# Performance work log

Hardware: AMD Instinct MI355X
Metric: run time of the kernel (lower is better)

Reference implementation:

```python
import jax, jax.numpy as jnp
import numpy as np
from jax import lax

DIM = 256
SEQ = 1024
BATCH = 4
EPS = 1e-6
P_TANH_SCALE = 10.0


def setup_inputs() -> dict:
    key = jax.random.key(0)
    ks = jax.random.split(key, 12)
    d, n, b = DIM, SEQ, BATCH
    half = d // 2
    x = jax.random.normal(ks[0], (b, n, d), jnp.float32)
    # RoPE frequencies (standard llama-style), complex freqs_cis split into cos/sin
    inv_freq = 1.0 / (10000.0 ** (np.arange(half, dtype=np.float64) * 2.0 / d))
    ang = np.outer(np.arange(n, dtype=np.float64), inv_freq)  # (n, d/2)
    freqs_cis_cos = jnp.asarray(np.cos(ang), jnp.float32)
    freqs_cis_sin = jnp.asarray(np.sin(ang), jnp.float32)
    s = 1.0 / np.sqrt(d)
    Wqkv = jax.random.normal(ks[1], (3 * d, d), jnp.float32) * s
    qconv_w = jax.random.normal(ks[2], (d, 4), jnp.float32) * 0.3
    qconv_b = jax.random.normal(ks[3], (d,), jnp.float32) * 0.02
    kconv_w = jax.random.normal(ks[4], (d, 4), jnp.float32) * 0.3
    kconv_b = jax.random.normal(ks[5], (d,), jnp.float32) * 0.02
    vconv_w = jax.random.normal(ks[6], (d, 4), jnp.float32) * 0.3
    vconv_b = jax.random.normal(ks[7], (d,), jnp.float32) * 0.02
    Wparam = jax.random.normal(ks[8], (2, d), jnp.float32) * s
    bparam = jnp.zeros((2,), jnp.float32)
    W0 = jnp.eye(d, dtype=jnp.float32)  # nn.init.eye_
    Wgate = jax.random.normal(ks[9], (d, d), jnp.float32) * s
    Wout = jax.random.normal(ks[10], (d, d), jnp.float32) * s
    return dict(x=x, freqs_cis_cos=freqs_cis_cos, freqs_cis_sin=freqs_cis_sin,
                Wqkv=Wqkv, qconv_w=qconv_w, qconv_b=qconv_b,
                kconv_w=kconv_w, kconv_b=kconv_b, vconv_w=vconv_w, vconv_b=vconv_b,
                Wparam=Wparam, bparam=bparam, W0=W0, Wgate=Wgate, Wout=Wout)


def _causal_dwconv(x, w, bias):
    # x: (b,n,d); w: (d,4); torch Conv1d(k=4, pad=3, groups=d) truncated to [:n]
    # y[t] = sum_j w[:,j] * x[t-3+j]  (zero left-pad)
    b, n, d = x.shape
    xp = jnp.pad(x, ((0, 0), (3, 0), (0, 0)))
    y = sum(xp[:, j:j + n, :] * w[None, None, :, j] for j in range(4))
    return y + bias[None, None, :]


def _rope(x, cos, sin):
    # x: (b,n,d); pairs (x[...,2i], x[...,2i+1]) rotated by freqs_cis
    xr, xi = x[..., 0::2], x[..., 1::2]
    c, s = cos[None], sin[None]
    outr = xr * c - xi * s
    outi = xr * s + xi * c
    return jnp.stack((outr, outi), axis=-1).reshape(x.shape)


def _l2norm(x):
    nrm = jnp.linalg.norm(x, axis=-1, keepdims=True)
    return x / jnp.maximum(nrm, 1e-12)


def _forward(x, cos, sin, Wqkv, qw, qb, kw, kb, vw, vb, Wparam, bparam, W0, Wgate, Wout):
    b, n, d = x.shape
    qkv = x @ Wqkv.T
    q, k, v = jnp.split(qkv, 3, axis=-1)
    q = _causal_dwconv(q, qw, qb)
    k = _causal_dwconv(k, kw, kb)
    v = _causal_dwconv(v, vw, vb)
    q = _l2norm(_rope(q, cos, sin))
    k = _l2norm(_rope(k, cos, sin))
    params = x @ Wparam.T + bparam  # (b,n,2)
    eta = jax.nn.sigmoid(params[..., 0])    # (b,n)
    alpha = jax.nn.sigmoid(params[..., 1])  # (b,n)

    def step(carry, inp):
        A, W = carry                      # (b,d,d)
        qt, kt, vt, et, at = inp          # (b,d)x3, (b,)x2
        pred = jnp.einsum('bd,bde->be', kt, W)
        diff = pred - vt
        grad_pred = 3.0 * jnp.tanh(P_TANH_SCALE * diff) * (diff * diff)  # p == 3
        grad_W = kt[:, :, None] * grad_pred[:, None, :]
        A = at[:, None, None] * A - et[:, None, None] * grad_W
        a4 = jnp.square(jnp.square(A))  # q == 4
        denom = jnp.sqrt(a4.sum(axis=(-2, -1), keepdims=True)) + EPS
        W = A / denom
        yt = jnp.einsum('bd,bde->be', qt, W)
        return (A, W), yt

    A0 = jnp.zeros((b, d, d), x.dtype)
    W_init = jnp.broadcast_to(W0, (b, d, d)).astype(x.dtype)
    xs = (q.transpose(1, 0, 2), k.transpose(1, 0, 2), v.transpose(1, 0, 2),
          eta.T, alpha.T)
    _, yT = lax.scan(jax.checkpoint(step), (A0, W_init), xs)
    y = yT.transpose(1, 0, 2)  # (b,n,d)
    return (y @ Wout.T) * jax.nn.sigmoid(x @ Wgate.T)


def reference(x, freqs_cis_cos, freqs_cis_sin, Wqkv, qconv_w, qconv_b,
              kconv_w, kconv_b, vconv_w, vconv_b, Wparam, bparam, W0, Wgate, Wout):
    return _forward(x, freqs_cis_cos, freqs_cis_sin, Wqkv, qconv_w, qconv_b,
                    kconv_w, kconv_b, vconv_w, vconv_b, Wparam, bparam, W0, Wgate, Wout)
```

## Files before the change

### kernel.cpp

```cpp
#include <hip/hip_runtime.h>

#define DIMD 256
#define SEQT 1024
#define NB   4
#define RBS  36

typedef float v2f __attribute__((ext_vector_type(2)));
#define FMA2(a,b,c) __builtin_elementwise_fma((a),(b),(c))

__device__ __forceinline__ float sigmoidf_(float x){ return 1.0f/(1.0f+expf(-x)); }

template<int EPI>
__global__ __launch_bounds__(256) void gemm_bt(const float* __restrict__ A,
    const float* __restrict__ Bm, float* __restrict__ C, int N,
    const float* __restrict__ gpre)
{
  __shared__ float sA[64][68];
  __shared__ float sB[64][68];
  const int nb = N >> 6;
  const int bm = blockIdx.x / nb, bn = blockIdx.x - bm*nb;
  const int m0 = bm << 6, n0 = bn << 6;
  const int tid = threadIdx.x;
  const int tr = tid >> 4, tc = tid & 15;
  float acc[4][4];
  #pragma unroll
  for (int i=0;i<4;i++)
    #pragma unroll
    for (int j=0;j<4;j++) acc[i][j]=0.f;

  for (int kc=0;kc<4;kc++){
    __syncthreads();
    for (int i=tid;i<1024;i+=256){
      int r = i >> 4, q4 = i & 15;
      *(float4*)&sA[r][q4*4] = ((const float4*)(A  + (m0+r)*256 + kc*64))[q4];
      *(float4*)&sB[r][q4*4] = ((const float4*)(Bm + (n0+r)*256 + kc*64))[q4];
    }
    __syncthreads();
    #pragma unroll
    for (int kq=0;kq<16;kq++){
      float4 av[4], bv[4];
      #pragma unroll
      for (int i=0;i<4;i++) av[i] = *(const float4*)&sA[tr+16*i][kq*4];
      #pragma unroll
      for (int j=0;j<4;j++) bv[j] = *(const float4*)&sB[tc+16*j][kq*4];
      #pragma unroll
      for (int i=0;i<4;i++)
        #pragma unroll
        for (int j=0;j<4;j++)
          acc[i][j] = fmaf(av[i].x,bv[j].x, fmaf(av[i].y,bv[j].y,
                      fmaf(av[i].z,bv[j].z, fmaf(av[i].w,bv[j].w, acc[i][j]))));
    }
  }
  #pragma unroll
  for (int i=0;i<4;i++){
    #pragma unroll
    for (int j=0;j<4;j++){
      int m = m0 + tr + 16*i, n = n0 + tc + 16*j;
      float val = acc[i][j];
      if (EPI==1) val *= sigmoidf_(gpre[m*N+n]);
      C[m*N+n] = val;
    }
  }
}

__global__ __launch_bounds__(256) void prep_kernel(
    const float* __restrict__ qkvr, const float* __restrict__ x,
    const float* __restrict__ cosT, const float* __restrict__ sinT,
    const float* __restrict__ qw, const float* __restrict__ qbias,
    const float* __restrict__ kw, const float* __restrict__ kbias,
    const float* __restrict__ vw, const float* __restrict__ vbias,
    const float* __restrict__ Wparam, const float* __restrict__ bparam,
    float* __restrict__ qo, float* __restrict__ ko, float* __restrict__ vo,
    float* __restrict__ eo, float* __restrict__ ao)
{
  const int bt = blockIdx.x;
  const int t = bt & 1023;
  const int d = threadIdx.x;

  float4 wq = ((const float4*)qw)[d];
  float4 wk = ((const float4*)kw)[d];
  float4 wv = ((const float4*)vw)[d];
  const float wqj[4] = {wq.x,wq.y,wq.z,wq.w};
  const float wkj[4] = {wk.x,wk.y,wk.z,wk.w};
  const float wvj[4] = {wv.x,wv.y,wv.z,wv.w};
  float qa = qbias[d], ka = kbias[d], va = vbias[d];
  #pragma unroll
  for (int j=0;j<4;j++){
    int tt = t - 3 + j;
    if (tt >= 0) {
      const float* row = qkvr + (size_t)(bt - 3 + j) * 768;
      qa = fmaf(row[d],      wqj[j], qa);
      ka = fmaf(row[256+d],  wkj[j], ka);
      va = fmaf(row[512+d],  wvj[j], va);
    }
  }
  vo[bt*256 + d] = va;

  __shared__ float sq[256], sk[256];
  __shared__ float red[4][4];
  sq[d] = qa; sk[d] = ka;
  __syncthreads();
  const int i = d >> 1;
  const float c = cosT[t*128 + i], s = sinT[t*128 + i];
  float qr, krp;
  if ((d & 1) == 0) { qr = sq[d]*c - sq[d+1]*s;  krp = sk[d]*c - sk[d+1]*s; }
  else              { qr = sq[d-1]*s + sq[d]*c;  krp = sk[d-1]*s + sk[d]*c; }

  const float xd = x[bt*256 + d];
  float r0 = qr*qr, r1 = krp*krp, r2 = xd*Wparam[d], r3 = xd*Wparam[256+d];
  #pragma unroll
  for (int m=1;m<64;m<<=1){
    r0 += __shfl_xor(r0, m, 64);
    r1 += __shfl_xor(r1, m, 64);
    r2 += __shfl_xor(r2, m, 64);
    r3 += __shfl_xor(r3, m, 64);
  }
  const int w = d >> 6;
  if ((d & 63) == 0){ red[w][0]=r0; red[w][1]=r1; red[w][2]=r2; red[w][3]=r3; }
  __syncthreads();
  float qss = red[0][0]+red[1][0]+red[2][0]+red[3][0];
  float kss = red[0][1]+red[1][1]+red[2][1]+red[3][1];
  qo[bt*256+d] = qr  / fmaxf(sqrtf(qss), 1e-12f);
  ko[bt*256+d] = krp / fmaxf(sqrtf(kss), 1e-12f);
  if (d == 0){
    float p0 = red[0][2]+red[1][2]+red[2][2]+red[3][2] + bparam[0];
    float p1 = red[0][3]+red[1][3]+red[2][3]+red[3][3] + bparam[1];
    eo[bt] = 1.f/(1.f+expf(-p0));
    ao[bt] = 1.f/(1.f+expf(-p1));
  }
}

__global__ __launch_bounds__(1024, 4) void scan_kernel(
    const float* __restrict__ qn, const float* __restrict__ kn,
    const float* __restrict__ vn, const float* __restrict__ eta,
    const float* __restrict__ alpha, const float* __restrict__ W0,
    float* __restrict__ y, float* __restrict__ g_s4)
{
  const int blkid = blockIdx.x;
  const int b     = blkid >> 1;
  const int h     = blkid & 1;
  const int peerb = blkid ^ 1;
  const int tid = threadIdx.x;
  const int rg = tid & 7;
  const int cl = tid >> 3;
  const int cg = (h << 7) + cl;
  const int r0 = rg << 5;
  const int koff = rg * RBS;

  __shared__ float s_k[3][8*RBS], s_q[3][8*RBS], s_v[3][256];
  __shared__ float s_ea[3][2];
  __shared__ float s_acc[4];
  __shared__ unsigned s_cnt[4];

  v2f A2[16];
  #pragma unroll
  for (int j=0;j<16;j++) A2[j] = (v2f)(0.f);

  const float* kb = kn + b*SEQT*DIMD;
  const float* qb = qn + b*SEQT*DIMD;
  const float* vb = vn + b*SEQT*DIMD;
  const float* eb = eta   + b*SEQT;
  const float* ab = alpha + b*SEQT;
  float* yb = y + b*SEQT*DIMD;

  if (tid < 4) { s_acc[tid] = 0.f; s_cnt[tid] = 0u; }

  if (tid < 64) {
    float4 v0 = ((const float4*)kb)[tid];
    *(float4*)&s_k[0][(tid>>3)*RBS + (tid&7)*4] = v0;
  } else if (tid < 128) {
    int i = tid-64;
    float4 v0 = ((const float4*)qb)[i];
    *(float4*)&s_q[0][(i>>3)*RBS + (i&7)*4] = v0;
  } else if (tid < 192) {
    ((float4*)s_v[0])[tid-128] = ((const float4*)vb)[tid-128];
  }
  if (tid == 192) { s_ea[0][0] = eb[0]; s_ea[0][1] = ab[0]; }

  float4 pf = make_float4(0.f,0.f,0.f,0.f);
  float pe = 0.f, pa = 0.f;
  if (tid < 64)       pf = ((const float4*)(kb + DIMD))[tid];
  else if (tid < 128) pf = ((const float4*)(qb + DIMD))[tid-64];
  else if (tid < 192) pf = ((const float4*)(vb + DIMD))[tid-128];
  if (tid == 192) { pe = eb[1]; pa = ab[1]; }
  __syncthreads();

  float pr = 0.f;
  {
    #pragma unroll 4
    for (int j=0;j<32;j++)
      pr = fmaf(s_k[0][koff + j], W0[(size_t)(r0+j)*DIMD + cg], pr);
    pr += __shfl_xor(pr, 1, 64);
    pr += __shfl_xor(pr, 2, 64);
    pr += __shfl_xor(pr, 4, 64);
  }

  float up = 0.f;
  int cur = 0;

  for (int t=0; t<SEQT; ++t) {
    const int nxt = (cur==2) ? 0 : cur+1;

    if (t+1 < SEQT) {
      if (tid < 64)       *(float4*)&s_k[nxt][(tid>>3)*RBS + (tid&7)*4] = pf;
      else if (tid < 128){ int i = tid-64; *(float4*)&s_q[nxt][(i>>3)*RBS + (i&7)*4] = pf; }
      else if (tid < 192) ((float4*)s_v[nxt])[tid-128] = pf;
      if (tid == 192) { s_ea[nxt][0]=pe; s_ea[nxt][1]=pa; }
    }

    __syncthreads();

    if (tid == 256) { s_acc[(t+1)&3] = 0.f; s_cnt[(t+1)&3] = 0u; }

    if (t+2 < SEQT) {
      if (tid < 64)       pf = ((const float4*)(kb + (t+2)*DIMD))[tid];
      else if (tid < 128) pf = ((const float4*)(qb + (t+2)*DIMD))[tid-64];
      else if (tid < 192) pf = ((const float4*)(vb + (t+2)*DIMD))[tid-128];
      if (tid == 192) { pe = eb[t+2]; pa = ab[t+2]; }
    }

    float scale = 1.f;
    if (t > 0) {
      float own = s_acc[(t-1)&3];
      const unsigned* pp = (const unsigned*)&g_s4[(size_t)(t-1)*8 + peerb];
      unsigned pv;
      do {
        pv = __hip_atomic_load(pp, __ATOMIC_ACQUIRE, __HIP_MEMORY_SCOPE_AGENT);
      } while (pv == 0xAAAAAAAAu);
      float s4t = own + __uint_as_float(pv);
      float w = sqrtf(s4t) + 1e-6f;
      float r = __builtin_amdgcn_rcpf(w);
      r = r * (2.f - w*r);
      scale = r;
      if (rg == 0) yb[(size_t)(t-1)*DIMD + cg] = up * r;
    }

    const float et = s_ea[cur][0], al = s_ea[cur][1];
    float pred = pr * scale;
    float df = pred - s_v[cur][cg];
    float e  = __expf(20.f*df);
    float th = 1.f - 2.f*__builtin_amdgcn_rcpf(e + 1.f);
    float t0 = et * 3.f * th * (df*df);
    v2f nt0; nt0.x = -t0; nt0.y = -t0;
    v2f alv; alv.x = al;  alv.y = al;

    const float4* kp = (const float4*)(s_k[cur] + koff);
    const float4* qp = (const float4*)(s_q[cur] + koff);
    const float4* np = (const float4*)(s_k[nxt] + koff);
    v2f s4v = (v2f)(0.f), uv = (v2f)(0.f), pv2 = (v2f)(0.f);
    #pragma unroll
    for (int j=0;j<8;j++){
      float4 k4 = kp[j], q4 = qp[j], n4 = np[j];
      v2f klo = {k4.x,k4.y}, khi = {k4.z,k4.w};
      v2f qlo = {q4.x,q4.y}, qhi = {q4.z,q4.w};
      v2f nlo = {n4.x,n4.y}, nhi = {n4.z,n4.w};
      v2f a, sq;
      a = FMA2(alv, A2[2*j],   nt0*klo); A2[2*j]   = a;
      sq = a*a; s4v = FMA2(sq, sq, s4v);
      uv  = FMA2(qlo, a, uv);
      pv2 = FMA2(nlo, a, pv2);
      a = FMA2(alv, A2[2*j+1], nt0*khi); A2[2*j+1] = a;
      sq = a*a; s4v = FMA2(sq, sq, s4v);
      uv  = FMA2(qhi, a, uv);
      pv2 = FMA2(nhi, a, pv2);
    }

    float u = uv.x + uv.y;
    float p = pv2.x + pv2.y;
    u += __shfl_xor(u, 1, 64); p += __shfl_xor(p, 1, 64);
    u += __shfl_xor(u, 2, 64); p += __shfl_xor(p, 2, 64);
    u += __shfl_xor(u, 4, 64); p += __shfl_xor(p, 4, 64);
    up = u; pr = p;

    float s4 = s4v.x + s4v.y;
    #pragma unroll
    for (int m=1;m<64;m<<=1) s4 += __shfl_xor(s4, m, 64);
    if ((tid & 63) == 0) {
      atomicAdd(&s_acc[t&3], s4);
      unsigned old = atomicAdd(&s_cnt[t&3], 1u);
      if (old == 15u) {
        float tot = s_acc[t&3];
        __hip_atomic_store((unsigned*)&g_s4[(size_t)t*8 + blkid],
                           __float_as_uint(tot),
                           __ATOMIC_RELEASE, __HIP_MEMORY_SCOPE_AGENT);
      }
    }

    cur = nxt;
  }

  __syncthreads();
  {
    float own = s_acc[1023&3];
    const unsigned* pp = (const unsigned*)&g_s4[(size_t)1023*8 + peerb];
    unsigned pv;
    do {
      pv = __hip_atomic_load(pp, __ATOMIC_ACQUIRE, __HIP_MEMORY_SCOPE_AGENT);
    } while (pv == 0xAAAAAAAAu);
    float s4t = own + __uint_as_float(pv);
    float w = sqrtf(s4t) + 1e-6f;
    float r = __builtin_amdgcn_rcpf(w);
    r = r * (2.f - w*r);
    if (rg == 0) yb[(size_t)1023*DIMD + cg] = up * r;
  }
}

extern "C" void kernel_launch(void* const* d_in, const int* in_sizes, int n_in,
                              void* d_out, int out_size, void* d_ws, size_t ws_size,
                              hipStream_t stream)
{
  const float* x     = (const float*)d_in[0];
  const float* cosT  = (const float*)d_in[1];
  const float* sinT  = (const float*)d_in[2];
  const float* Wqkv  = (const float*)d_in[3];
  const float* qw    = (const float*)d_in[4];
  const float* qb    = (const float*)d_in[5];
  const float* kw    = (const float*)d_in[6];
  const float* kb    = (const float*)d_in[7];
  const float* vw    = (const float*)d_in[8];
  const float* vb    = (const float*)d_in[9];
  const float* Wparam= (const float*)d_in[10];
  const float* bparam= (const float*)d_in[11];
  const float* W0    = (const float*)d_in[12];
  const float* Wgate = (const float*)d_in[13];
  const float* Wout  = (const float*)d_in[14];
  float* out = (float*)d_out;

  float* ws    = (float*)d_ws;
  float* qkvr  = ws;
  float* qn    = qkvr + 4*1024*768;
  float* kn    = qn   + 4*1024*256;
  float* vn    = kn   + 4*1024*256;
  float* eta   = vn   + 4*1024*256;
  float* alpha = eta  + 4096;
  float* yv    = qkvr;
  float* tmpg  = qkvr + 1048576;
  float* g_s4  = qkvr + 2097152;

  gemm_bt<0><<<dim3(64*12), 256, 0, stream>>>(x, Wqkv, qkvr, 768, nullptr);
  prep_kernel<<<dim3(4096), 256, 0, stream>>>(qkvr, x, cosT, sinT,
      qw, qb, kw, kb, vw, vb, Wparam, bparam, qn, kn, vn, eta, alpha);
  hipMemsetAsync(g_s4, 0xAA, (size_t)SEQT*8*sizeof(float), stream);
  scan_kernel<<<dim3(NB*2), 1024, 0, stream>>>(qn, kn, vn, eta, alpha, W0,
                                               yv, g_s4);
  gemm_bt<0><<<dim3(64*4), 256, 0, stream>>>(x, Wgate, tmpg, 256, nullptr);
  gemm_bt<1><<<dim3(64*4), 256, 0, stream>>>(yv, Wout, out, 256, tmpg);
}
```

Baseline: 3.131 ms.

## Replace LDS-then-global two-level reduction with direct global atomic sum and counter

The per-step sum-of-fourth-powers reduction across the two cooperating blocks now has every wave atomically add its partial into a per-timestep global float and bump a global counter with release ordering. Readers spin until the counter reaches 32. This removes the LDS atomics, the last-wave publish step and the sentinel-value polling, and it issues the reduction before the u/p shuffles so it overlaps with them. In exchange, 32 waves now contend on global atomics every step, the float atomicAdd order becomes nondeterministic, and the launch attributes are rewritten as explicit amdgpu attributes.

```diff
diff --git a/kernel.cpp b/kernel.cpp
--- a/kernel.cpp
+++ b/kernel.cpp
@@ -130,16 +130,18 @@
   }
 }
 
-__global__ __launch_bounds__(1024, 4) void scan_kernel(
+__global__ void __attribute__((amdgpu_flat_work_group_size(1024,1024),
+                               amdgpu_waves_per_eu(4,4)))
+scan_kernel(
     const float* __restrict__ qn, const float* __restrict__ kn,
     const float* __restrict__ vn, const float* __restrict__ eta,
     const float* __restrict__ alpha, const float* __restrict__ W0,
-    float* __restrict__ y, float* __restrict__ g_s4)
+    float* __restrict__ y, float* __restrict__ g_sum,
+    unsigned* __restrict__ g_cnt)
 {
   const int blkid = blockIdx.x;
   const int b     = blkid >> 1;
   const int h     = blkid & 1;
-  const int peerb = blkid ^ 1;
   const int tid = threadIdx.x;
   const int rg = tid & 7;
   const int cl = tid >> 3;
@@ -149,8 +151,6 @@
 
   __shared__ float s_k[3][8*RBS], s_q[3][8*RBS], s_v[3][256];
   __shared__ float s_ea[3][2];
-  __shared__ float s_acc[4];
-  __shared__ unsigned s_cnt[4];
 
   v2f A2[16];
   #pragma unroll
@@ -162,8 +162,8 @@
   const float* eb = eta   + b*SEQT;
   const float* ab = alpha + b*SEQT;
   float* yb = y + b*SEQT*DIMD;
-
-  if (tid < 4) { s_acc[tid] = 0.f; s_cnt[tid] = 0u; }
+  float*    sumb = g_sum + b*SEQT;
+  unsigned* cntb = g_cnt + b*SEQT;
 
   if (tid < 64) {
     float4 v0 = ((const float4*)kb)[tid];
@@ -210,8 +210,6 @@
 
     __syncthreads();
 
-    if (tid == 256) { s_acc[(t+1)&3] = 0.f; s_cnt[(t+1)&3] = 0u; }
-
     if (t+2 < SEQT) {
       if (tid < 64)       pf = ((const float4*)(kb + (t+2)*DIMD))[tid];
       else if (tid < 128) pf = ((const float4*)(qb + (t+2)*DIMD))[tid-64];
@@ -221,13 +219,9 @@
 
     float scale = 1.f;
     if (t > 0) {
-      float own = s_acc[(t-1)&3];
-      const unsigned* pp = (const unsigned*)&g_s4[(size_t)(t-1)*8 + peerb];
-      unsigned pv;
-      do {
-        pv = __hip_atomic_load(pp, __ATOMIC_ACQUIRE, __HIP_MEMORY_SCOPE_AGENT);
-      } while (pv == 0xAAAAAAAAu);
-      float s4t = own + __uint_as_float(pv);
+      while (__hip_atomic_load(&cntb[t-1], __ATOMIC_ACQUIRE,
+                               __HIP_MEMORY_SCOPE_AGENT) != 32u) {}
+      float s4t = sumb[t-1];
       float w = sqrtf(s4t) + 1e-6f;
       float r = __builtin_amdgcn_rcpf(w);
       r = r * (2.f - w*r);
@@ -265,6 +259,15 @@
       pv2 = FMA2(nhi, a, pv2);
     }
 
+    float s4 = s4v.x + s4v.y;
+    #pragma unroll
+    for (int m=1;m<64;m<<=1) s4 += __shfl_xor(s4, m, 64);
+    if ((tid & 63) == 0) {
+      atomicAdd(&sumb[t], s4);
+      __hip_atomic_fetch_add(&cntb[t], 1u,
+                             __ATOMIC_RELEASE, __HIP_MEMORY_SCOPE_AGENT);
+    }
+
     float u = uv.x + uv.y;
     float p = pv2.x + pv2.y;
     u += __shfl_xor(u, 1, 64); p += __shfl_xor(p, 1, 64);
@@ -272,36 +275,17 @@
     u += __shfl_xor(u, 4, 64); p += __shfl_xor(p, 4, 64);
     up = u; pr = p;
 
-    float s4 = s4v.x + s4v.y;
-    #pragma unroll
-    for (int m=1;m<64;m<<=1) s4 += __shfl_xor(s4, m, 64);
-    if ((tid & 63) == 0) {
-      atomicAdd(&s_acc[t&3], s4);
-      unsigned old = atomicAdd(&s_cnt[t&3], 1u);
-      if (old == 15u) {
-        float tot = s_acc[t&3];
-        __hip_atomic_store((unsigned*)&g_s4[(size_t)t*8 + blkid],
-                           __float_as_uint(tot),
-                           __ATOMIC_RELEASE, __HIP_MEMORY_SCOPE_AGENT);
-      }
-    }
-
     cur = nxt;
   }
 
-  __syncthreads();
   {
-    float own = s_acc[1023&3];
-    const unsigned* pp = (const unsigned*)&g_s4[(size_t)1023*8 + peerb];
-    unsigned pv;
-    do {
-      pv = __hip_atomic_load(pp, __ATOMIC_ACQUIRE, __HIP_MEMORY_SCOPE_AGENT);
-    } while (pv == 0xAAAAAAAAu);
-    float s4t = own + __uint_as_float(pv);
+    while (__hip_atomic_load(&cntb[SEQT-1], __ATOMIC_ACQUIRE,
+                             __HIP_MEMORY_SCOPE_AGENT) != 32u) {}
+    float s4t = sumb[SEQT-1];
     float w = sqrtf(s4t) + 1e-6f;
     float r = __builtin_amdgcn_rcpf(w);
     r = r * (2.f - w*r);
-    if (rg == 0) yb[(size_t)1023*DIMD + cg] = up * r;
+    if (rg == 0) yb[(size_t)(SEQT-1)*DIMD + cg] = up * r;
   }
 }
 
@@ -335,14 +319,15 @@
   float* alpha = eta  + 4096;
   float* yv    = qkvr;
   float* tmpg  = qkvr + 1048576;
-  float* g_s4  = qkvr + 2097152;
+  float* g_sum = qkvr + 2097152;
+  unsigned* g_cnt = (unsigned*)(qkvr + 2097152 + 4096);
 
   gemm_bt<0><<<dim3(64*12), 256, 0, stream>>>(x, Wqkv, qkvr, 768, nullptr);
   prep_kernel<<<dim3(4096), 256, 0, stream>>>(qkvr, x, cosT, sinT,
       qw, qb, kw, kb, vw, vb, Wparam, bparam, qn, kn, vn, eta, alpha);
-  hipMemsetAsync(g_s4, 0xAA, (size_t)SEQT*8*sizeof(float), stream);
+  hipMemsetAsync(g_sum, 0, (size_t)8192*sizeof(float), stream);
   scan_kernel<<<dim3(NB*2), 1024, 0, stream>>>(qn, kn, vn, eta, alpha, W0,
-                                               yv, g_s4);
+                                               yv, g_sum, g_cnt);
   gemm_bt<0><<<dim3(64*4), 256, 0, stream>>>(x, Wgate, tmpg, 256, nullptr);
   gemm_bt<1><<<dim3(64*4), 256, 0, stream>>>(yv, Wout, out, 256, tmpg);
 }
```

New measurement: 5.351 ms. 1.71x slower.
